# Optimization experiments

Hardware: AMD Instinct MI355X
Metric: run time of the kernel (lower is better)

Reference implementation:

```python
import jax, jax.numpy as jnp
import numpy as np

HEAD_DIM = 64
SCALE = 1.0 / np.sqrt(HEAD_DIM).astype(np.float32)


def setup_inputs() -> dict:
    key = jax.random.key(0)
    k1, k2 = jax.random.split(key)
    B, S, D = 4, 4096, 1024
    x = jax.random.normal(k1, (B, S, D), dtype=jnp.float32)
    wq = jax.random.normal(k2, (HEAD_DIM, D), dtype=jnp.float32) * (1.0 / np.sqrt(D))
    return {"x": x, "wq": wq}


def reference(x, wq):
    # Faithful to the original forward: wq is (buggily) used for q, k AND v.
    q = jnp.einsum('bsd,hd->bsh', x, wq)   # [B, S, 64]
    k = q
    v = q
    scores = jnp.einsum('bqh,bkh->bqk', q, k) * SCALE  # [B, S, S]
    attn = jax.nn.softmax(scores, axis=-1)
    out = jnp.einsum('bqk,bkh->bqh', attn, v)          # [B, S, 64]
    return out
```

## Files before the change

kernel.cpp:

```cpp
#include <hip/hip_runtime.h>
#include <hip/hip_bf16.h>

#define B_ 4
#define S_ 4096
#define D_ 1024
#define H_ 64
#define SCALE_ 0.125f
#define WP_ 1056
#define SP_ 4224

typedef __attribute__((ext_vector_type(8))) short bf16x8;
typedef __attribute__((ext_vector_type(4))) short bf16x4;
typedef __attribute__((ext_vector_type(4))) float f32x4;

static __device__ __forceinline__ short f2bf(float f) {
    unsigned u = __builtin_bit_cast(unsigned, f);
    u += 0x7fffu + ((u >> 16) & 1u);
    return (short)(u >> 16);
}

__global__ __launch_bounds__(256) void winit_kernel(
    const float* __restrict__ wq, short* __restrict__ wqb)
{
    const int i   = blockIdx.x * 256 + threadIdx.x;
    const int row = i >> 7;
    const int col = (i & 127) * 8;
    const float* s = wq + (size_t)row * D_ + col;
    bf16x8 v;
#pragma unroll
    for (int e = 0; e < 8; ++e) v[e] = f2bf(s[e]);
    *(bf16x8*)(wqb + (size_t)row * WP_ + col) = v;
}

__global__ __launch_bounds__(256) void qproj_mfma(
    const float* __restrict__ x, const short* __restrict__ wqb,
    short* __restrict__ q, short* __restrict__ qT)
{
    __shared__ short xs[4][16][264];
    __shared__ float cs[4][16][68];
    __shared__ short qs[16][68];

    const int tid  = threadIdx.x;
    const int wave = tid >> 6;
    const int lane = tid & 63;
    const int quad = lane >> 4;
    const int lr   = lane & 15;
    const int row0 = blockIdx.x * 16;

    {
        const float* xp = x + (size_t)row0 * D_ + wave * 256 + lane * 4;
#pragma unroll
        for (int s = 0; s < 16; ++s) {
            const f32x4 v = *(const f32x4*)(xp + (size_t)s * D_);
            unsigned long long pk = 0;
#pragma unroll
            for (int e = 0; e < 4; ++e)
                pk |= (unsigned long long)(unsigned short)f2bf(v[e]) << (16 * e);
            *(unsigned long long*)&xs[wave][s][lane * 4] = pk;
        }
    }
    __syncthreads();

    f32x4 acc[4];
#pragma unroll
    for (int nb = 0; nb < 4; ++nb) acc[nb] = (f32x4){0.f, 0.f, 0.f, 0.f};

    const short* wp = wqb + (size_t)lr * WP_ + wave * 256 + quad * 8;
#pragma unroll
    for (int t = 0; t < 8; ++t) {
        const bf16x8 a = *(const bf16x8*)&xs[wave][lr][t * 32 + quad * 8];
#pragma unroll
        for (int nb = 0; nb < 4; ++nb) {
            const bf16x8 bb = *(const bf16x8*)(wp + (size_t)(nb * 16) * WP_ + t * 32);
            acc[nb] = __builtin_amdgcn_mfma_f32_16x16x32_bf16(a, bb, acc[nb], 0, 0, 0);
        }
    }

#pragma unroll
    for (int nb = 0; nb < 4; ++nb)
#pragma unroll
        for (int i = 0; i < 4; ++i)
            cs[wave][quad * 4 + i][nb * 16 + lr] = acc[nb][i];
    __syncthreads();

    const int r  = tid >> 4;
    const int c4 = (tid & 15) * 4;
    unsigned long long pv = 0;
#pragma unroll
    for (int j = 0; j < 4; ++j) {
        const float s = cs[0][r][c4 + j] + cs[1][r][c4 + j]
                      + cs[2][r][c4 + j] + cs[3][r][c4 + j];
        pv |= (unsigned long long)(unsigned short)f2bf(s) << (16 * j);
    }
    *(unsigned long long*)(q + (size_t)(row0 + r) * H_ + c4) = pv;
    *(unsigned long long*)&qs[r][c4] = pv;
    __syncthreads();

    const int hh = tid >> 2;
    const int sj = (tid & 3) * 4;
    const int b  = row0 >> 12;
    const int sl = row0 & (S_ - 1);
    unsigned long long w = 0;
#pragma unroll
    for (int e = 0; e < 4; ++e)
        w |= (unsigned long long)(unsigned short)qs[sj + e][hh] << (16 * e);
    *(unsigned long long*)(qT + ((size_t)b * H_ + hh) * SP_ + sl + sj) = w;
}

__global__ __launch_bounds__(256, 4) void flash_mfma(
    const short* __restrict__ q, const short* __restrict__ qT,
    float* __restrict__ opart, float* __restrict__ lbuf)
{
    __shared__ short kt[64][72];
    __shared__ short vt[64][72];
    __shared__ short plT[4][16][72];

    const int tid  = threadIdx.x;
    const int w    = tid >> 6;
    const int lane = tid & 63;
    const int quad = lane >> 4;
    const int lr   = lane & 15;
    const int b    = blockIdx.y;
    const int q0   = blockIdx.x * 64;
    const int z    = blockIdx.z;
    const int slice = S_ / gridDim.z;
    const int kbase = z * slice;
    const short* qb  = q  + (size_t)b * S_ * H_;
    const short* qTb = qT + (size_t)b * H_ * SP_;

    bf16x8 qB[2];
    {
        const short* qr = qb + (size_t)(q0 + w * 16 + lr) * H_;
        qB[0] = *(const bf16x8*)(qr + quad * 8);
        qB[1] = *(const bf16x8*)(qr + 32 + quad * 8);
    }

    f32x4 o[4];
#pragma unroll
    for (int mt = 0; mt < 4; ++mt) o[mt] = (f32x4){0.f, 0.f, 0.f, 0.f};
    float lacc = 0.0f;

    const int srow = tid >> 2;
    const int scol = (tid & 3) * 16;
    const short* gk = qb  + (size_t)(kbase + srow) * H_ + scol;
    const short* gv = qTb + (size_t)srow * SP_ + kbase + scol;

    uint4 pk0 = *(const uint4*)gk, pk1 = *(const uint4*)(gk + 8);
    uint4 pv0 = *(const uint4*)gv, pv1 = *(const uint4*)(gv + 8);

    const int iters = slice >> 6;
    for (int it = 0; it < iters; ++it) {
        __syncthreads();
        *(uint4*)&kt[srow][scol]     = pk0;
        *(uint4*)&kt[srow][scol + 8] = pk1;
        *(uint4*)&vt[srow][scol]     = pv0;
        *(uint4*)&vt[srow][scol + 8] = pv1;
        __syncthreads();
        if (it + 1 < iters) {
            gk += (size_t)64 * H_;
            gv += 64;
            pk0 = *(const uint4*)gk; pk1 = *(const uint4*)(gk + 8);
            pv0 = *(const uint4*)gv; pv1 = *(const uint4*)(gv + 8);
        }

        f32x4 s[4];
#pragma unroll
        for (int mt = 0; mt < 4; ++mt) s[mt] = (f32x4){0.f, 0.f, 0.f, 0.f};
#pragma unroll
        for (int c = 0; c < 2; ++c)
#pragma unroll
            for (int mt = 0; mt < 4; ++mt) {
                const bf16x8 a = *(const bf16x8*)&kt[mt * 16 + lr][c * 32 + quad * 8];
                s[mt] = __builtin_amdgcn_mfma_f32_16x16x32_bf16(a, qB[c], s[mt], 0, 0, 0);
            }

#pragma unroll
        for (int mt = 0; mt < 4; ++mt) {
            bf16x4 pb;
#pragma unroll
            for (int i = 0; i < 4; ++i) {
                const float p = __expf(s[mt][i] * SCALE_);
                lacc += p;
                pb[i] = f2bf(p);
            }
            *(bf16x4*)&plT[w][lr][mt * 16 + quad * 4] = pb;
        }

#pragma unroll
        for (int c = 0; c < 2; ++c) {
            const bf16x8 pB = *(const bf16x8*)&plT[w][lr][c * 32 + quad * 8];
#pragma unroll
            for (int mt = 0; mt < 4; ++mt) {
                const bf16x8 a = *(const bf16x8*)&vt[mt * 16 + lr][c * 32 + quad * 8];
                o[mt] = __builtin_amdgcn_mfma_f32_16x16x32_bf16(a, pB, o[mt], 0, 0, 0);
            }
        }
    }

    lacc += __shfl_xor(lacc, 16, 64);
    lacc += __shfl_xor(lacc, 32, 64);

    float* ob = opart + (((size_t)z * B_ + b) * S_ + q0 + w * 16 + lr) * H_;
#pragma unroll
    for (int mt = 0; mt < 4; ++mt)
        *(f32x4*)(ob + mt * 16 + quad * 4) = o[mt];
    if (quad == 0)
        lbuf[((size_t)z * B_ + b) * S_ + q0 + w * 16 + lr] = lacc;
}

__global__ __launch_bounds__(256) void combine_kernel(
    const float* __restrict__ opart, const float* __restrict__ lbuf,
    float* __restrict__ out, int nsplit)
{
    const int t   = blockIdx.x * 256 + threadIdx.x;
    const int row = t >> 4;
    const int c4  = (t & 15) * 4;
    f32x4 acc = (f32x4){0.f, 0.f, 0.f, 0.f};
    float l = 0.0f;
    for (int z = 0; z < nsplit; ++z) {
        const f32x4 v = *(const f32x4*)(opart + ((size_t)z * (B_ * S_) + row) * H_ + c4);
        acc[0] += v[0]; acc[1] += v[1]; acc[2] += v[2]; acc[3] += v[3];
        l += lbuf[(size_t)z * (B_ * S_) + row];
    }
    const float r = 1.0f / l;
    acc[0] *= r; acc[1] *= r; acc[2] *= r; acc[3] *= r;
    *(f32x4*)(out + (size_t)row * H_ + c4) = acc;
}

extern "C" void kernel_launch(void* const* d_in, const int* in_sizes, int n_in,
                              void* d_out, int out_size, void* d_ws, size_t ws_size,
                              hipStream_t stream) {
    const float* x  = (const float*)d_in[0];
    const float* wq = (const float*)d_in[1];
    float* out = (float*)d_out;

    const size_t off_qT  = 2097152;
    const size_t off_wqb = off_qT + (size_t)B_ * H_ * SP_ * 2;
    const size_t off_op  = off_wqb + (size_t)H_ * WP_ * 2;
    short* qbuf = (short*)d_ws;
    short* qT   = (short*)((char*)d_ws + off_qT);
    short* wqb  = (short*)((char*)d_ws + off_wqb);

    const size_t per_split = (size_t)B_ * S_ * H_ * 4 + (size_t)B_ * S_ * 4;
    int nsplit = 4;
    if (ws_size < off_op + 4 * per_split) nsplit = 1;
    float* opart = (float*)((char*)d_ws + off_op);
    float* lbuf  = (float*)((char*)d_ws + off_op + (size_t)nsplit * B_ * S_ * H_ * 4);

    winit_kernel<<<dim3(32), dim3(256), 0, stream>>>(wq, wqb);
    qproj_mfma<<<dim3((B_ * S_) / 16), dim3(256), 0, stream>>>(x, wqb, qbuf, qT);
    flash_mfma<<<dim3(S_ / 64, B_, nsplit), dim3(256), 0, stream>>>(qbuf, qT, opart, lbuf);
    combine_kernel<<<dim3(1024), dim3(256), 0, stream>>>(opart, lbuf, out, nsplit);
}
```

Before: 138.6 us.

## Double query rows per wave, swizzle K/V LDS, and raise KV split count

Each wave now handles two 16-row query sets, so every K/V fragment read from LDS feeds two MFMAs, and the block covers 128 query rows. The padded K/V LDS tiles are replaced by unpadded 64x64 tiles with an XOR swizzle to avoid bank conflicts. The KV split count rises from 4 to 8 when workspace allows, which keeps the grid size unchanged. The cost is more accumulator registers per thread, which may lower occupancy, plus larger partial buffers and more work in the combine kernel.

```diff
diff --git a/kernel.cpp b/kernel.cpp
--- a/kernel.cpp
+++ b/kernel.cpp
@@ -8,6 +8,7 @@
 #define SCALE_ 0.125f
 #define WP_ 1056
 #define SP_ 4224
+#define NSPLIT 8
 
 typedef __attribute__((ext_vector_type(8))) short bf16x8;
 typedef __attribute__((ext_vector_type(4))) short bf16x4;
@@ -111,9 +112,9 @@
     const short* __restrict__ q, const short* __restrict__ qT,
     float* __restrict__ opart, float* __restrict__ lbuf)
 {
-    __shared__ short kt[64][72];
-    __shared__ short vt[64][72];
-    __shared__ short plT[4][16][72];
+    __shared__ short kt[64 * 64];
+    __shared__ short vt[64 * 64];
+    __shared__ short plT[4][2][16][72];
 
     const int tid  = threadIdx.x;
     const int w    = tid >> 6;
@@ -121,29 +122,34 @@
     const int quad = lane >> 4;
     const int lr   = lane & 15;
     const int b    = blockIdx.y;
-    const int q0   = blockIdx.x * 64;
+    const int q0   = blockIdx.x * 128;
     const int z    = blockIdx.z;
     const int slice = S_ / gridDim.z;
     const int kbase = z * slice;
     const short* qb  = q  + (size_t)b * S_ * H_;
     const short* qTb = qT + (size_t)b * H_ * SP_;
 
-    bf16x8 qB[2];
-    {
-        const short* qr = qb + (size_t)(q0 + w * 16 + lr) * H_;
-        qB[0] = *(const bf16x8*)(qr + quad * 8);
-        qB[1] = *(const bf16x8*)(qr + 32 + quad * 8);
-    }
-
-    f32x4 o[4];
-#pragma unroll
-    for (int mt = 0; mt < 4; ++mt) o[mt] = (f32x4){0.f, 0.f, 0.f, 0.f};
-    float lacc = 0.0f;
+    bf16x8 qB[2][2];
+#pragma unroll
+    for (int set = 0; set < 2; ++set) {
+        const short* qr = qb + (size_t)(q0 + w * 32 + set * 16 + lr) * H_;
+        qB[set][0] = *(const bf16x8*)(qr + quad * 8);
+        qB[set][1] = *(const bf16x8*)(qr + 32 + quad * 8);
+    }
+
+    f32x4 o[2][4];
+#pragma unroll
+    for (int set = 0; set < 2; ++set)
+#pragma unroll
+        for (int mt = 0; mt < 4; ++mt) o[set][mt] = (f32x4){0.f, 0.f, 0.f, 0.f};
+    float lacc[2] = {0.f, 0.f};
 
     const int srow = tid >> 2;
-    const int scol = (tid & 3) * 16;
-    const short* gk = qb  + (size_t)(kbase + srow) * H_ + scol;
-    const short* gv = qTb + (size_t)srow * SP_ + kbase + scol;
+    const int g0   = (tid & 3) * 2;
+    const int sw0  = (g0 ^ (srow & 7)) * 8;
+    const int sw1  = ((g0 + 1) ^ (srow & 7)) * 8;
+    const short* gk = qb  + (size_t)(kbase + srow) * H_ + g0 * 8;
+    const short* gv = qTb + (size_t)srow * SP_ + kbase + g0 * 8;
 
     uint4 pk0 = *(const uint4*)gk, pk1 = *(const uint4*)(gk + 8);
     uint4 pv0 = *(const uint4*)gv, pv1 = *(const uint4*)(gv + 8);
@@ -151,10 +157,10 @@
     const int iters = slice >> 6;
     for (int it = 0; it < iters; ++it) {
         __syncthreads();
-        *(uint4*)&kt[srow][scol]     = pk0;
-        *(uint4*)&kt[srow][scol + 8] = pk1;
-        *(uint4*)&vt[srow][scol]     = pv0;
-        *(uint4*)&vt[srow][scol + 8] = pv1;
+        *(uint4*)&kt[srow * 64 + sw0] = pk0;
+        *(uint4*)&kt[srow * 64 + sw1] = pk1;
+        *(uint4*)&vt[srow * 64 + sw0] = pv0;
+        *(uint4*)&vt[srow * 64 + sw1] = pv1;
         __syncthreads();
         if (it + 1 < iters) {
             gk += (size_t)64 * H_;
@@ -163,49 +169,61 @@
             pv0 = *(const uint4*)gv; pv1 = *(const uint4*)(gv + 8);
         }
 
-        f32x4 s[4];
-#pragma unroll
-        for (int mt = 0; mt < 4; ++mt) s[mt] = (f32x4){0.f, 0.f, 0.f, 0.f};
+        f32x4 s[2][4];
+#pragma unroll
+        for (int set = 0; set < 2; ++set)
+#pragma unroll
+            for (int mt = 0; mt < 4; ++mt) s[set][mt] = (f32x4){0.f, 0.f, 0.f, 0.f};
 #pragma unroll
         for (int c = 0; c < 2; ++c)
 #pragma unroll
             for (int mt = 0; mt < 4; ++mt) {
-                const bf16x8 a = *(const bf16x8*)&kt[mt * 16 + lr][c * 32 + quad * 8];
-                s[mt] = __builtin_amdgcn_mfma_f32_16x16x32_bf16(a, qB[c], s[mt], 0, 0, 0);
+                const int row = mt * 16 + lr;
+                const bf16x8 a = *(const bf16x8*)&kt[row * 64 + (((c * 4 + quad) ^ (row & 7)) * 8)];
+                s[0][mt] = __builtin_amdgcn_mfma_f32_16x16x32_bf16(a, qB[0][c], s[0][mt], 0, 0, 0);
+                s[1][mt] = __builtin_amdgcn_mfma_f32_16x16x32_bf16(a, qB[1][c], s[1][mt], 0, 0, 0);
             }
 
 #pragma unroll
-        for (int mt = 0; mt < 4; ++mt) {
-            bf16x4 pb;
-#pragma unroll
-            for (int i = 0; i < 4; ++i) {
-                const float p = __expf(s[mt][i] * SCALE_);
-                lacc += p;
-                pb[i] = f2bf(p);
+        for (int set = 0; set < 2; ++set)
+#pragma unroll
+            for (int mt = 0; mt < 4; ++mt) {
+                bf16x4 pb;
+#pragma unroll
+                for (int i = 0; i < 4; ++i) {
+                    const float p = __expf(s[set][mt][i] * SCALE_);
+                    lacc[set] += p;
+                    pb[i] = f2bf(p);
+                }
+                *(bf16x4*)&plT[w][set][lr][mt * 16 + quad * 4] = pb;
             }
-            *(bf16x4*)&plT[w][lr][mt * 16 + quad * 4] = pb;
-        }
 
 #pragma unroll
         for (int c = 0; c < 2; ++c) {
-            const bf16x8 pB = *(const bf16x8*)&plT[w][lr][c * 32 + quad * 8];
+            const bf16x8 pB0 = *(const bf16x8*)&plT[w][0][lr][c * 32 + quad * 8];
+            const bf16x8 pB1 = *(const bf16x8*)&plT[w][1][lr][c * 32 + quad * 8];
 #pragma unroll
             for (int mt = 0; mt < 4; ++mt) {
-                const bf16x8 a = *(const bf16x8*)&vt[mt * 16 + lr][c * 32 + quad * 8];
-                o[mt] = __builtin_amdgcn_mfma_f32_16x16x32_bf16(a, pB, o[mt], 0, 0, 0);
+                const int row = mt * 16 + lr;
+                const bf16x8 a = *(const bf16x8*)&vt[row * 64 + (((c * 4 + quad) ^ (row & 7)) * 8)];
+                o[0][mt] = __builtin_amdgcn_mfma_f32_16x16x32_bf16(a, pB0, o[0][mt], 0, 0, 0);
+                o[1][mt] = __builtin_amdgcn_mfma_f32_16x16x32_bf16(a, pB1, o[1][mt], 0, 0, 0);
             }
         }
     }
 
-    lacc += __shfl_xor(lacc, 16, 64);
-    lacc += __shfl_xor(lacc, 32, 64);
-
-    float* ob = opart + (((size_t)z * B_ + b) * S_ + q0 + w * 16 + lr) * H_;
-#pragma unroll
-    for (int mt = 0; mt < 4; ++mt)
-        *(f32x4*)(ob + mt * 16 + quad * 4) = o[mt];
-    if (quad == 0)
-        lbuf[((size_t)z * B_ + b) * S_ + q0 + w * 16 + lr] = lacc;
+#pragma unroll
+    for (int set = 0; set < 2; ++set) {
+        float v = lacc[set];
+        v += __shfl_xor(v, 16, 64);
+        v += __shfl_xor(v, 32, 64);
+        float* ob = opart + (((size_t)z * B_ + b) * S_ + q0 + w * 32 + set * 16 + lr) * H_;
+#pragma unroll
+        for (int mt = 0; mt < 4; ++mt)
+            *(f32x4*)(ob + mt * 16 + quad * 4) = o[set][mt];
+        if (quad == 0)
+            lbuf[((size_t)z * B_ + b) * S_ + q0 + w * 32 + set * 16 + lr] = v;
+    }
 }
 
 __global__ __launch_bounds__(256) void combine_kernel(
@@ -242,13 +260,13 @@
     short* wqb  = (short*)((char*)d_ws + off_wqb);
 
     const size_t per_split = (size_t)B_ * S_ * H_ * 4 + (size_t)B_ * S_ * 4;
-    int nsplit = 4;
-    if (ws_size < off_op + 4 * per_split) nsplit = 1;
+    int nsplit = NSPLIT;
+    while (nsplit > 1 && ws_size < off_op + (size_t)nsplit * per_split) nsplit >>= 1;
     float* opart = (float*)((char*)d_ws + off_op);
     float* lbuf  = (float*)((char*)d_ws + off_op + (size_t)nsplit * B_ * S_ * H_ * 4);
 
     winit_kernel<<<dim3(32), dim3(256), 0, stream>>>(wq, wqb);
     qproj_mfma<<<dim3((B_ * S_) / 16), dim3(256), 0, stream>>>(x, wqb, qbuf, qT);
-    flash_mfma<<<dim3(S_ / 64, B_, nsplit), dim3(256), 0, stream>>>(qbuf, qT, opart, lbuf);
+    flash_mfma<<<dim3(S_ / 128, B_, nsplit), dim3(256), 0, stream>>>(qbuf, qT, opart, lbuf);
     combine_kernel<<<dim3(1024), dim3(256), 0, stream>>>(opart, lbuf, out, nsplit);
 }
```

After: 148.0 us. 1.07x slower.

## Prescale Q by log2e*scale, swizzle LDS tiles, compute row sums via MFMA

Applied to the files above, without the earlier changes.

The projection kernel now also writes a copy of Q premultiplied by scale*log2(e). The attention loop can then use raw exp2 instead of a multiply plus expf. K and V tiles move to an XOR-swizzled, unpadded LDS layout to avoid bank conflicts. The softmax denominator is accumulated with an extra MFMA against a vector of ones instead of scalar adds and shuffles, and probabilities are packed to bf16 by truncation rather than rounding. The cost is an extra Q buffer write/read and slightly different rounding in P and the row sums.

```diff
diff --git a/kernel.cpp b/kernel.cpp
--- a/kernel.cpp
+++ b/kernel.cpp
@@ -6,17 +6,23 @@
 #define D_ 1024
 #define H_ 64
 #define SCALE_ 0.125f
+#define CFAC_ 0.180336884f
 #define WP_ 1056
 #define SP_ 4224
+#define NSPLIT 4
 
 typedef __attribute__((ext_vector_type(8))) short bf16x8;
-typedef __attribute__((ext_vector_type(4))) short bf16x4;
 typedef __attribute__((ext_vector_type(4))) float f32x4;
 
 static __device__ __forceinline__ short f2bf(float f) {
     unsigned u = __builtin_bit_cast(unsigned, f);
     u += 0x7fffu + ((u >> 16) & 1u);
     return (short)(u >> 16);
+}
+
+static __device__ __forceinline__ unsigned pk_trunc(float f0, float f1) {
+    return (__builtin_bit_cast(unsigned, f1) & 0xffff0000u)
+         | (__builtin_bit_cast(unsigned, f0) >> 16);
 }
 
 __global__ __launch_bounds__(256) void winit_kernel(
@@ -34,7 +40,7 @@
 
 __global__ __launch_bounds__(256) void qproj_mfma(
     const float* __restrict__ x, const short* __restrict__ wqb,
-    short* __restrict__ q, short* __restrict__ qT)
+    short* __restrict__ q, short* __restrict__ qT, short* __restrict__ qsb)
 {
     __shared__ short xs[4][16][264];
     __shared__ float cs[4][16][68];
@@ -85,14 +91,16 @@
 
     const int r  = tid >> 4;
     const int c4 = (tid & 15) * 4;
-    unsigned long long pv = 0;
+    unsigned long long pv = 0, pw = 0;
 #pragma unroll
     for (int j = 0; j < 4; ++j) {
         const float s = cs[0][r][c4 + j] + cs[1][r][c4 + j]
                       + cs[2][r][c4 + j] + cs[3][r][c4 + j];
         pv |= (unsigned long long)(unsigned short)f2bf(s) << (16 * j);
-    }
-    *(unsigned long long*)(q + (size_t)(row0 + r) * H_ + c4) = pv;
+        pw |= (unsigned long long)(unsigned short)f2bf(s * CFAC_) << (16 * j);
+    }
+    *(unsigned long long*)(q   + (size_t)(row0 + r) * H_ + c4) = pv;
+    *(unsigned long long*)(qsb + (size_t)(row0 + r) * H_ + c4) = pw;
     *(unsigned long long*)&qs[r][c4] = pv;
     __syncthreads();
 
@@ -109,10 +117,11 @@
 
 __global__ __launch_bounds__(256, 4) void flash_mfma(
     const short* __restrict__ q, const short* __restrict__ qT,
+    const short* __restrict__ qsb,
     float* __restrict__ opart, float* __restrict__ lbuf)
 {
-    __shared__ short kt[64][72];
-    __shared__ short vt[64][72];
+    __shared__ short kt[64 * 64];
+    __shared__ short vt[64 * 64];
     __shared__ short plT[4][16][72];
 
     const int tid  = threadIdx.x;
@@ -130,20 +139,26 @@
 
     bf16x8 qB[2];
     {
-        const short* qr = qb + (size_t)(q0 + w * 16 + lr) * H_;
+        const short* qr = qsb + (size_t)(b * S_ + q0 + w * 16 + lr) * H_;
         qB[0] = *(const bf16x8*)(qr + quad * 8);
         qB[1] = *(const bf16x8*)(qr + 32 + quad * 8);
     }
 
+    bf16x8 ones;
+#pragma unroll
+    for (int e = 0; e < 8; ++e) ones[e] = (short)0x3f80;
+
     f32x4 o[4];
 #pragma unroll
     for (int mt = 0; mt < 4; ++mt) o[mt] = (f32x4){0.f, 0.f, 0.f, 0.f};
-    float lacc = 0.0f;
+    f32x4 lsum = (f32x4){0.f, 0.f, 0.f, 0.f};
 
     const int srow = tid >> 2;
-    const int scol = (tid & 3) * 16;
-    const short* gk = qb  + (size_t)(kbase + srow) * H_ + scol;
-    const short* gv = qTb + (size_t)srow * SP_ + kbase + scol;
+    const int g0   = (tid & 3) * 2;
+    const int sw0  = (g0 ^ (srow & 7)) * 8;
+    const int sw1  = ((g0 + 1) ^ (srow & 7)) * 8;
+    const short* gk = qb  + (size_t)(kbase + srow) * H_ + g0 * 8;
+    const short* gv = qTb + (size_t)srow * SP_ + kbase + g0 * 8;
 
     uint4 pk0 = *(const uint4*)gk, pk1 = *(const uint4*)(gk + 8);
     uint4 pv0 = *(const uint4*)gv, pv1 = *(const uint4*)(gv + 8);
@@ -151,10 +166,10 @@
     const int iters = slice >> 6;
     for (int it = 0; it < iters; ++it) {
         __syncthreads();
-        *(uint4*)&kt[srow][scol]     = pk0;
-        *(uint4*)&kt[srow][scol + 8] = pk1;
-        *(uint4*)&vt[srow][scol]     = pv0;
-        *(uint4*)&vt[srow][scol + 8] = pv1;
+        *(uint4*)&kt[srow * 64 + sw0] = pk0;
+        *(uint4*)&kt[srow * 64 + sw1] = pk1;
+        *(uint4*)&vt[srow * 64 + sw0] = pv0;
+        *(uint4*)&vt[srow * 64 + sw1] = pv1;
         __syncthreads();
         if (it + 1 < iters) {
             gk += (size_t)64 * H_;
@@ -170,42 +185,43 @@
         for (int c = 0; c < 2; ++c)
 #pragma unroll
             for (int mt = 0; mt < 4; ++mt) {
-                const bf16x8 a = *(const bf16x8*)&kt[mt * 16 + lr][c * 32 + quad * 8];
+                const int row = mt * 16 + lr;
+                const bf16x8 a = *(const bf16x8*)&kt[row * 64 + (((c * 4 + quad) ^ (row & 7)) * 8)];
                 s[mt] = __builtin_amdgcn_mfma_f32_16x16x32_bf16(a, qB[c], s[mt], 0, 0, 0);
             }
 
 #pragma unroll
         for (int mt = 0; mt < 4; ++mt) {
-            bf16x4 pb;
-#pragma unroll
-            for (int i = 0; i < 4; ++i) {
-                const float p = __expf(s[mt][i] * SCALE_);
-                lacc += p;
-                pb[i] = f2bf(p);
-            }
-            *(bf16x4*)&plT[w][lr][mt * 16 + quad * 4] = pb;
+            const float p0 = __builtin_amdgcn_exp2f(s[mt][0]);
+            const float p1 = __builtin_amdgcn_exp2f(s[mt][1]);
+            const float p2 = __builtin_amdgcn_exp2f(s[mt][2]);
+            const float p3 = __builtin_amdgcn_exp2f(s[mt][3]);
+            unsigned lohi[2];
+            lohi[0] = pk_trunc(p0, p1);
+            lohi[1] = pk_trunc(p2, p3);
+            *(unsigned long long*)&plT[w][lr][mt * 16 + quad * 4] =
+                *(unsigned long long*)lohi;
         }
 
 #pragma unroll
         for (int c = 0; c < 2; ++c) {
             const bf16x8 pB = *(const bf16x8*)&plT[w][lr][c * 32 + quad * 8];
+            lsum = __builtin_amdgcn_mfma_f32_16x16x32_bf16(ones, pB, lsum, 0, 0, 0);
 #pragma unroll
             for (int mt = 0; mt < 4; ++mt) {
-                const bf16x8 a = *(const bf16x8*)&vt[mt * 16 + lr][c * 32 + quad * 8];
+                const int row = mt * 16 + lr;
+                const bf16x8 a = *(const bf16x8*)&vt[row * 64 + (((c * 4 + quad) ^ (row & 7)) * 8)];
                 o[mt] = __builtin_amdgcn_mfma_f32_16x16x32_bf16(a, pB, o[mt], 0, 0, 0);
             }
         }
     }
-
-    lacc += __shfl_xor(lacc, 16, 64);
-    lacc += __shfl_xor(lacc, 32, 64);
 
     float* ob = opart + (((size_t)z * B_ + b) * S_ + q0 + w * 16 + lr) * H_;
 #pragma unroll
     for (int mt = 0; mt < 4; ++mt)
         *(f32x4*)(ob + mt * 16 + quad * 4) = o[mt];
     if (quad == 0)
-        lbuf[((size_t)z * B_ + b) * S_ + q0 + w * 16 + lr] = lacc;
+        lbuf[((size_t)z * B_ + b) * S_ + q0 + w * 16 + lr] = lsum[0];
 }
 
 __global__ __launch_bounds__(256) void combine_kernel(
@@ -236,19 +252,21 @@
 
     const size_t off_qT  = 2097152;
     const size_t off_wqb = off_qT + (size_t)B_ * H_ * SP_ * 2;
-    const size_t off_op  = off_wqb + (size_t)H_ * WP_ * 2;
+    const size_t off_qsb = off_wqb + (size_t)H_ * WP_ * 2;
+    const size_t off_op  = off_qsb + 2097152;
     short* qbuf = (short*)d_ws;
     short* qT   = (short*)((char*)d_ws + off_qT);
     short* wqb  = (short*)((char*)d_ws + off_wqb);
+    short* qsb  = (short*)((char*)d_ws + off_qsb);
 
     const size_t per_split = (size_t)B_ * S_ * H_ * 4 + (size_t)B_ * S_ * 4;
-    int nsplit = 4;
-    if (ws_size < off_op + 4 * per_split) nsplit = 1;
+    int nsplit = NSPLIT;
+    while (nsplit > 1 && ws_size < off_op + (size_t)nsplit * per_split) nsplit >>= 1;
     float* opart = (float*)((char*)d_ws + off_op);
     float* lbuf  = (float*)((char*)d_ws + off_op + (size_t)nsplit * B_ * S_ * H_ * 4);
 
     winit_kernel<<<dim3(32), dim3(256), 0, stream>>>(wq, wqb);
-    qproj_mfma<<<dim3((B_ * S_) / 16), dim3(256), 0, stream>>>(x, wqb, qbuf, qT);
-    flash_mfma<<<dim3(S_ / 64, B_, nsplit), dim3(256), 0, stream>>>(qbuf, qT, opart, lbuf);
+    qproj_mfma<<<dim3((B_ * S_) / 16), dim3(256), 0, stream>>>(x, wqb, qbuf, qT, qsb);
+    flash_mfma<<<dim3(S_ / 64, B_, nsplit), dim3(256), 0, stream>>>(qbuf, qT, qsb, opart, lbuf);
     combine_kernel<<<dim3(1024), dim3(256), 0, stream>>>(opart, lbuf, out, nsplit);
 }
```

New measurement: 134.3 us. -3.1%, faster.
